# Performance work log

Measured on AMD Instinct MI355X. Metric: run time of the kernel, lower is better.

## Reference

```python
import jax, jax.numpy as jnp
import numpy as np

B, H, W, C, HEADS, WS, SS = 32, 56, 56, 512, 16, 7, 3
HID = 4 * C
N = WS * WS          # tokens per window = 49
NW = (H // WS) * (W // WS)  # windows per image = 64
HD = C // HEADS
SCALE = HD ** -0.5

def _rel_index():
    coords = np.stack(np.meshgrid(np.arange(WS), np.arange(WS), indexing='ij'))
    cf = coords.reshape(2, -1)
    rel = (cf[:, :, None] - cf[:, None, :]).transpose(1, 2, 0)
    rel[..., 0] += WS - 1
    rel[..., 1] += WS - 1
    rel[..., 0] *= 2 * WS - 1
    return rel.sum(-1)  # [N, N]

REL_IDX = _rel_index()

def _attn_mask():
    # standard Swin SW-MSA mask: label 3x3 shifted regions, diff labels -> -100
    img = np.zeros((H, W), dtype=np.float32)
    cnt = 0
    for hs in (slice(0, -WS), slice(-WS, -SS), slice(-SS, None)):
        for ws_ in (slice(0, -WS), slice(-WS, -SS), slice(-SS, None)):
            img[hs, ws_] = cnt
            cnt += 1
    mw = img.reshape(H // WS, WS, W // WS, WS).transpose(0, 2, 1, 3).reshape(NW, N)
    diff = mw[:, None, :] - mw[:, :, None]
    return jnp.asarray(np.where(diff != 0, -100.0, 0.0).astype(np.float32))  # [NW, N, N]

ATTN_MASK = _attn_mask()

def layernorm(x, g, b, eps=1e-5):
    m = jnp.mean(x, -1, keepdims=True)
    v = jnp.mean((x - m) ** 2, -1, keepdims=True)
    return (x - m) * jax.lax.rsqrt(v + eps) * g + b

def setup_inputs():
    key = jax.random.key(0)
    ks = jax.random.split(key, 8)
    f32 = jnp.float32
    return {
        'x': jax.random.normal(ks[0], (B, H * W, C), f32),
        'norm1_g': jnp.ones((C,), f32), 'norm1_b': jnp.zeros((C,), f32),
        'qkv_w': jax.random.normal(ks[1], (3 * C, C), f32) * 0.02,
        'qkv_b': jnp.zeros((3 * C,), f32),
        'rel_bias': jax.random.normal(ks[2], ((2 * WS - 1) ** 2, HEADS), f32) * 0.02,
        'proj_w': jax.random.normal(ks[3], (C, C), f32) * 0.02,
        'proj_b': jnp.zeros((C,), f32),
        'norm2_g': jnp.ones((C,), f32), 'norm2_b': jnp.zeros((C,), f32),
        'mlp_w1': jax.random.normal(ks[4], (HID, C), f32) * 0.02,
        'mlp_b1': jnp.zeros((HID,), f32),
        'mlp_w2': jax.random.normal(ks[5], (C, HID), f32) * 0.02,
        'mlp_b2': jnp.zeros((C,), f32),
    }

def reference(x, norm1_g, norm1_b, qkv_w, qkv_b, rel_bias, proj_w, proj_b,
              norm2_g, norm2_b, mlp_w1, mlp_b1, mlp_w2, mlp_b2):
    skip = x
    h = layernorm(x, norm1_g, norm1_b).reshape(B, H, W, C)
    h = jnp.roll(h, (-SS, -SS), axis=(1, 2))  # cyclic shift
    # window partition -> [B*NW, N, C]
    h = h.reshape(B, H // WS, WS, W // WS, WS, C).transpose(0, 1, 3, 2, 4, 5).reshape(B * NW, N, C)
    qkv = (h @ qkv_w.T + qkv_b).reshape(B * NW, N, 3, HEADS, HD).transpose(2, 0, 3, 1, 4)
    q, k, v = qkv[0] * SCALE, qkv[1], qkv[2]  # [B*NW, HEADS, N, HD]
    attn = jnp.einsum('whnd,whmd->whnm', q, k)
    bias = rel_bias[REL_IDX.reshape(-1)].reshape(N, N, HEADS).transpose(2, 0, 1)
    attn = attn + bias[None]
    attn = attn.reshape(B, NW, HEADS, N, N) + ATTN_MASK[None, :, None]
    attn = jax.nn.softmax(attn, axis=-1).reshape(B * NW, HEADS, N, N)
    h = jnp.einsum('whnm,whmd->whnd', attn, v).transpose(0, 2, 1, 3).reshape(B * NW, N, C)
    h = h @ proj_w.T + proj_b
    # window reverse + reverse cyclic shift
    h = h.reshape(B, H // WS, W // WS, WS, WS, C).transpose(0, 1, 3, 2, 4, 5).reshape(B, H, W, C)
    h = jnp.roll(h, (SS, SS), axis=(1, 2)).reshape(B, H * W, C)
    x = skip + h
    m = layernorm(x, norm2_g, norm2_b)
    m = jax.nn.gelu(m @ mlp_w1.T + mlp_b1, approximate=False) @ mlp_w2.T + mlp_b2
    return x + m
```

## Files before the change

### kernel.cpp

```cpp
#include <hip/hip_runtime.h>
#include <cstdint>
#include <cstddef>

#define DI __device__ __forceinline__

typedef __bf16 bf16_t;
typedef __bf16 bf16x8 __attribute__((ext_vector_type(8)));
typedef float f32x4 __attribute__((ext_vector_type(4)));

static constexpr float SCALE = 0.17677669529663687f;

DI bf16_t f2b(float f) {
  uint32_t u = __builtin_bit_cast(uint32_t, f);
  u += 0x7fffu + ((u >> 16) & 1u);
  return __builtin_bit_cast(bf16_t, (uint16_t)(u >> 16));
}

DI void gld16(const void* g, void* l) {
  __builtin_amdgcn_global_load_lds(
      (const __attribute__((address_space(1))) uint32_t*)g,
      (__attribute__((address_space(3))) uint32_t*)l, 16, 0, 0);
}

__global__ __launch_bounds__(256)
void cvtw(const float* __restrict__ in, bf16_t* __restrict__ out, int n) {
  int i = (blockIdx.x * 256 + threadIdx.x) * 4;
  if (i >= n) return;
  float4 v = *(const float4*)(in + i);
  ushort4 o;
  o.x = __builtin_bit_cast(uint16_t, f2b(v.x));
  o.y = __builtin_bit_cast(uint16_t, f2b(v.y));
  o.z = __builtin_bit_cast(uint16_t, f2b(v.z));
  o.w = __builtin_bit_cast(uint16_t, f2b(v.w));
  *(ushort4*)(out + i) = o;
}

__global__ __launch_bounds__(256)
void bias_pre(const float* __restrict__ rel, float* __restrict__ bf) {
  int idx = blockIdx.x * 256 + threadIdx.x;
  int head = idx >> 12, t1 = (idx >> 6) & 63, t2 = idx & 63;
  float v = -1e30f;
  if (t1 < 49 && t2 < 49) {
    int i1 = t1 / 7, j1 = t1 - i1 * 7, i2 = t2 / 7, j2 = t2 - i2 * 7;
    v = rel[((i1 - i2 + 6) * 13 + (j1 - j2 + 6)) * 16 + head];
  }
  bf[idx] = v;
}

template<bool WIN>
__global__ __launch_bounds__(256)
void ln_kernel(const float* __restrict__ in, const float* __restrict__ g,
               const float* __restrict__ be, bf16_t* __restrict__ out)
{
  const int tid = threadIdx.x;
  const int r = blockIdx.x * 2 + (tid >> 7);
  const int ti = tid & 127;
  long srow;
  if (WIN) {
    int bw = r / 49, t = r - bw * 49;
    int b = bw >> 6, w = bw & 63;
    int wh = w >> 3, ww = w & 7;
    int i = t / 7, j = t - i * 7;
    int hs = wh * 7 + i + 3; if (hs >= 56) hs -= 56;
    int wsr = ww * 7 + j + 3; if (wsr >= 56) wsr -= 56;
    srow = (long)b * 3136 + hs * 56 + wsr;
  } else {
    srow = r;
  }
  const float4 v = *(const float4*)(in + srow * 512 + ti * 4);
  float s = v.x + v.y + v.z + v.w;
  float sq = v.x * v.x + v.y * v.y + v.z * v.z + v.w * v.w;
#pragma unroll
  for (int m = 1; m < 64; m <<= 1) { s += __shfl_xor(s, m); sq += __shfl_xor(sq, m); }
  __shared__ float ls[4], lq[4];
  const int wv = tid >> 6;
  if ((tid & 63) == 0) { ls[wv] = s; lq[wv] = sq; }
  __syncthreads();
  const int rp = (tid >> 7) * 2;
  s = ls[rp] + ls[rp + 1]; sq = lq[rp] + lq[rp + 1];
  const float mean = s * (1.f / 512.f);
  const float rs = rsqrtf(sq * (1.f / 512.f) - mean * mean + 1e-5f);
  const float4 gg = *(const float4*)(g + ti * 4);
  const float4 bb = *(const float4*)(be + ti * 4);
  ushort4 o;
  o.x = __builtin_bit_cast(uint16_t, f2b((v.x - mean) * rs * gg.x + bb.x));
  o.y = __builtin_bit_cast(uint16_t, f2b((v.y - mean) * rs * gg.y + bb.y));
  o.z = __builtin_bit_cast(uint16_t, f2b((v.z - mean) * rs * gg.z + bb.z));
  o.w = __builtin_bit_cast(uint16_t, f2b((v.w - mean) * rs * gg.w + bb.w));
  *(ushort4*)(out + (long)r * 512 + ti * 4) = o;
}

#define MFMA16(a, b, c) __builtin_amdgcn_mfma_f32_16x16x32_bf16((a), (b), (c), 0, 0, 0)

template<int EPI>
DI void epi_store(int grow, int gcol, float v, const float* extra,
                  void* out0, void* out1v, void* out2v)
{
  long obase = 0;
  if (EPI == 0) {
    int bwi = grow / 49, t_ = grow - bwi * 49;
    obase = ((long)bwi * 784 + t_) * 32;
  } else if (EPI == 1) {
    int bwi = grow / 49, t_ = grow - bwi * 49;
    int b = bwi >> 6, w = bwi & 63;
    int wh = w >> 3, ww = w & 7;
    int i = t_ / 7, jj = t_ - i * 7;
    int hs = wh * 7 + i + 3; if (hs >= 56) hs -= 56;
    int wsr = ww * 7 + jj + 3; if (wsr >= 56) wsr -= 56;
    obase = ((long)b * 3136 + hs * 56 + wsr) * 512;
  } else if (EPI == 2) {
    obase = (long)grow * 2048;
  } else {
    obase = (long)grow * 512;
  }
  if (EPI == 0) {
    int part = gcol >> 9, head = (gcol >> 5) & 15, d = gcol & 31;
    if (part == 0) v *= SCALE;
    bf16_t* dst = (bf16_t*)(part == 0 ? out0 : (part == 1 ? out1v : out2v));
    dst[obase + (long)head * 1568 + d] = f2b(v);
  } else if (EPI == 1) {
    ((float*)out0)[obase + gcol] = v + extra[obase + gcol];
  } else if (EPI == 2) {
    float m2 = v * v;
    float z = v * fmaf(0.07135481627f, m2, 1.59576912161f);
    float e = __expf(z);
    float rr = __builtin_amdgcn_rcpf(e + 1.0f);
    ((bf16_t*)out0)[obase + gcol] = f2b(fmaf(-v, rr, v));
  } else {
    ((float*)out0)[obase + gcol] = v + extra[obase + gcol];
  }
}

template<int EPI, int NBN, int NT>
__global__ __launch_bounds__(512, 2)
void gemmM(const bf16_t* __restrict__ A, const bf16_t* __restrict__ Bw,
           const float* __restrict__ bias, const float* __restrict__ extra,
           void* __restrict__ out0, void* __restrict__ out1v, void* __restrict__ out2v)
{
  constexpr int K = NT * 32;
  __shared__ __align__(128) bf16_t ldsA[2][8192];
  __shared__ __align__(128) bf16_t ldsB[4][8192];
  const int tid = threadIdx.x, lane = tid & 63, wave = tid >> 6;
  const int xcd = blockIdx.x & 7, j = blockIdx.x >> 3;
  const int m0 = xcd * 49;
  constexpr int ntileX = 49 * NBN;
  const int tiles = (ntileX - j + 31) >> 5;

  const int arow = tid >> 1, ac = (tid & 1) * 2;
  const int awb0 = arow * 64 + ((ac ^ ((arow >> 1) & 3)) << 4);
  const int awb1 = arow * 64 + (((ac + 1) ^ ((arow >> 1) & 3)) << 4);
  const int bsrow = tid >> 2;
  const int bchunk = (tid & 3) ^ ((bsrow >> 1) & 3);

  int ktS = 0, tS = j;
  const bf16_t* pA = A + ((size_t)(m0 + tS / NBN) * 256 + arow) * K + ac * 8;
  const bf16_t* pB = Bw + ((size_t)(tS % NBN) * 256 + bsrow) * K + bchunk * 8;

  struct QA { uint4 x, y; };
  QA qa0, qa1, qa2, qa3;

#define ADV() do { \
    if (++ktS == NT) { \
      ktS = 0; tS += 32; if (tS >= ntileX) tS = j; \
      pA = A + ((size_t)(m0 + tS / NBN) * 256 + arow) * K + ac * 8; \
      pB = Bw + ((size_t)(tS % NBN) * 256 + bsrow) * K + bchunk * 8; \
    } \
  } while (0)

#define STEPOPS(QI, TGT) do { \
    QI.x = *(const uint4*)(pA + ktS * 32); \
    QI.y = *(const uint4*)(pA + ktS * 32 + 8); \
    gld16(pB + ktS * 32, &ldsB[TGT][tid * 8]); \
    gld16(pB + ktS * 32 + (size_t)128 * K, &ldsB[TGT][tid * 8 + 4096]); \
    ADV(); \
  } while (0)

#define COMMIT(QC, BUF) do { \
    *(uint4*)((char*)&ldsA[BUF][0] + awb0) = QC.x; \
    *(uint4*)((char*)&ldsA[BUF][0] + awb1) = QC.y; \
  } while (0)

  const int fr = lane & 15, fkc = lane >> 4;
  const int wr = wave >> 2, wc = wave & 3;
  const int slotq = (fkc ^ ((fr >> 1) & 3)) << 3;
  const int aoff = (wr * 128 + fr) * 32 + slotq;
  const int boff = (wc * 64 + fr) * 32 + slotq;

  f32x4 acc[8][4] = {};

  STEPOPS(qa0, 0); STEPOPS(qa1, 1); STEPOPS(qa2, 2);
  asm volatile("s_waitcnt vmcnt(8)");
  __builtin_amdgcn_sched_barrier(0);
  COMMIT(qa0, 0);
  asm volatile("s_waitcnt lgkmcnt(0)");
  __builtin_amdgcn_s_barrier();
  __builtin_amdgcn_sched_barrier(0);

#define PH(P, QI, QC) do { \
    bf16x8 bq0 = *(const bf16x8*)&ldsB[(P) & 3][boff]; \
    bf16x8 bq1 = *(const bf16x8*)&ldsB[(P) & 3][boff + 512]; \
    bf16x8 bq2 = *(const bf16x8*)&ldsB[(P) & 3][boff + 1024]; \
    bf16x8 bq3 = *(const bf16x8*)&ldsB[(P) & 3][boff + 1536]; \
    bf16x8 a0 = *(const bf16x8*)&ldsA[(P) & 1][aoff]; \
    bf16x8 a1 = *(const bf16x8*)&ldsA[(P) & 1][aoff + 512]; \
    bf16x8 a2 = *(const bf16x8*)&ldsA[(P) & 1][aoff + 1024]; \
    bf16x8 a3 = *(const bf16x8*)&ldsA[(P) & 1][aoff + 1536]; \
    STEPOPS(QI, ((P) + 3) & 3); \
    asm volatile("s_waitcnt lgkmcnt(0)"); \
    __builtin_amdgcn_sched_barrier(0); \
    __builtin_amdgcn_s_setprio(1); \
    acc[0][0] = MFMA16(a0, bq0, acc[0][0]); acc[0][1] = MFMA16(a0, bq1, acc[0][1]); \
    acc[0][2] = MFMA16(a0, bq2, acc[0][2]); acc[0][3] = MFMA16(a0, bq3, acc[0][3]); \
    acc[1][0] = MFMA16(a1, bq0, acc[1][0]); acc[1][1] = MFMA16(a1, bq1, acc[1][1]); \
    acc[1][2] = MFMA16(a1, bq2, acc[1][2]); acc[1][3] = MFMA16(a1, bq3, acc[1][3]); \
    acc[2][0] = MFMA16(a2, bq0, acc[2][0]); acc[2][1] = MFMA16(a2, bq1, acc[2][1]); \
    acc[2][2] = MFMA16(a2, bq2, acc[2][2]); acc[2][3] = MFMA16(a2, bq3, acc[2][3]); \
    acc[3][0] = MFMA16(a3, bq0, acc[3][0]); acc[3][1] = MFMA16(a3, bq1, acc[3][1]); \
    acc[3][2] = MFMA16(a3, bq2, acc[3][2]); acc[3][3] = MFMA16(a3, bq3, acc[3][3]); \
    a0 = *(const bf16x8*)&ldsA[(P) & 1][aoff + 2048]; \
    a1 = *(const bf16x8*)&ldsA[(P) & 1][aoff + 2560]; \
    a2 = *(const bf16x8*)&ldsA[(P) & 1][aoff + 3072]; \
    a3 = *(const bf16x8*)&ldsA[(P) & 1][aoff + 3584]; \
    asm volatile("s_waitcnt lgkmcnt(0)"); \
    __builtin_amdgcn_sched_barrier(0); \
    acc[4][0] = MFMA16(a0, bq0, acc[4][0]); acc[4][1] = MFMA16(a0, bq1, acc[4][1]); \
    acc[4][2] = MFMA16(a0, bq2, acc[4][2]); acc[4][3] = MFMA16(a0, bq3, acc[4][3]); \
    acc[5][0] = MFMA16(a1, bq0, acc[5][0]); acc[5][1] = MFMA16(a1, bq1, acc[5][1]); \
    acc[5][2] = MFMA16(a1, bq2, acc[5][2]); acc[5][3] = MFMA16(a1, bq3, acc[5][3]); \
    acc[6][0] = MFMA16(a2, bq0, acc[6][0]); acc[6][1] = MFMA16(a2, bq1, acc[6][1]); \
    acc[6][2] = MFMA16(a2, bq2, acc[6][2]); acc[6][3] = MFMA16(a2, bq3, acc[6][3]); \
    acc[7][0] = MFMA16(a3, bq0, acc[7][0]); acc[7][1] = MFMA16(a3, bq1, acc[7][1]); \
    acc[7][2] = MFMA16(a3, bq2, acc[7][2]); acc[7][3] = MFMA16(a3, bq3, acc[7][3]); \
    __builtin_amdgcn_s_setprio(0); \
    __builtin_amdgcn_sched_barrier(0); \
    asm volatile("s_waitcnt vmcnt(8)"); \
    __builtin_amdgcn_sched_barrier(0); \
    COMMIT(QC, ((P) + 1) & 1); \
    asm volatile("s_waitcnt lgkmcnt(0)"); \
    __builtin_amdgcn_s_barrier(); \
    __builtin_amdgcn_sched_barrier(0); \
  } while (0)

  const int rq = fkc * 4;

  for (int t = 0; t < tiles; ++t) {
    const int tauC = j + t * 32;
    const int bmC = m0 + tauC / NBN;
    const int bnC = tauC % NBN;
#pragma unroll 1
    for (int it = 0; it < NT / 4; ++it) {
      PH(0, qa3, qa1);
      PH(1, qa0, qa2);
      PH(2, qa1, qa3);
      PH(3, qa2, qa0);
    }
    float bs[4];
#pragma unroll
    for (int n = 0; n < 4; ++n) bs[n] = bias[bnC * 256 + wc * 64 + n * 16 + fr];
#pragma unroll
    for (int m = 0; m < 8; ++m)
#pragma unroll
      for (int jj = 0; jj < 4; ++jj) {
        const int grow = bmC * 256 + wr * 128 + m * 16 + rq + jj;
#pragma unroll
        for (int n = 0; n < 4; ++n) {
          const int gcol = bnC * 256 + wc * 64 + n * 16 + fr;
          epi_store<EPI>(grow, gcol, acc[m][n][jj] + bs[n], extra, out0, out1v, out2v);
        }
      }
#pragma unroll
    for (int m = 0; m < 8; ++m)
#pragma unroll
      for (int n = 0; n < 4; ++n) acc[m][n] = (f32x4){0.f, 0.f, 0.f, 0.f};
  }
#undef PH
#undef COMMIT
#undef STEPOPS
#undef ADV
}

__global__ __launch_bounds__(256)
void attn_kernel(const bf16_t* __restrict__ qb, const bf16_t* __restrict__ kb,
                 const bf16_t* __restrict__ vb, const float* __restrict__ biasf,
                 bf16_t* __restrict__ aout)
{
  __shared__ bf16_t Q[64 * 32];
  __shared__ bf16_t Kl[64 * 32];
  __shared__ bf16_t Vt[32 * 64];
  __shared__ bf16_t Pl[4][16 * 64];
  const int bid = blockIdx.x;
  const int bw = bid >> 4, head = bid & 15;
  const int tid = threadIdx.x, lane = tid & 63, wave = tid >> 6;
  {
    uint4 z = {0u, 0u, 0u, 0u};
    *(uint4*)&Q[tid * 8] = z;
    *(uint4*)&Kl[tid * 8] = z;
    *(uint4*)&Vt[tid * 8] = z;
  }
  __syncthreads();
  const bf16_t* qsrc = qb + (long)bid * (49 * 32);
  const bf16_t* ksrc = kb + (long)bid * (49 * 32);
  const bf16_t* vsrc = vb + (long)bid * (49 * 32);
  if (tid < 196) {
    *(uint4*)&Q[tid * 8] = *(const uint4*)(qsrc + tid * 8);
    *(uint4*)&Kl[tid * 8] = *(const uint4*)(ksrc + tid * 8);
  }
  for (int e = tid; e < 1568; e += 256) {
    int t = e >> 5, d = e & 31;
    Vt[d * 64 + t] = vsrc[e];
  }
  __syncthreads();
  const int fr = lane & 15, fk = (lane >> 4) * 8, rq = (lane >> 4) * 4;
  bf16x8 aq = *(const bf16x8*)&Q[(wave * 16 + fr) * 32 + fk];
  f32x4 s[4];
#pragma unroll
  for (int n = 0; n < 4; ++n) {
    bf16x8 bk = *(const bf16x8*)&Kl[(n * 16 + fr) * 32 + fk];
    f32x4 z = {0.f, 0.f, 0.f, 0.f};
    s[n] = __builtin_amdgcn_mfma_f32_16x16x32_bf16(aq, bk, z, 0, 0, 0);
  }
  const int w = bw & 63;
  const bool wh7 = ((w >> 3) == 7), ww7 = ((w & 7) == 7);
  const float* bh = biasf + head * 4096;
#pragma unroll
  for (int j = 0; j < 4; ++j) {
    const int row = wave * 16 + rq + j;
    int i1 = row / 7, j1 = row - i1 * 7;
    bool b1h = wh7 && (i1 >= 4), b1w = ww7 && (j1 >= 4);
    float pv[4];
    float mx = -3.0e38f;
#pragma unroll
    for (int n = 0; n < 4; ++n) {
      const int col = n * 16 + fr;
      float v = s[n][j] + bh[row * 64 + col];
      if (wh7 || ww7) {
        int i2 = col / 7, j2 = col - i2 * 7;
        bool b2h = wh7 && (i2 >= 4), b2w = ww7 && (j2 >= 4);
        if ((b1h != b2h) || (b1w != b2w)) v -= 100.f;
      }
      pv[n] = v;
      mx = fmaxf(mx, v);
    }
#pragma unroll
    for (int msk = 1; msk < 16; msk <<= 1) mx = fmaxf(mx, __shfl_xor(mx, msk));
    float sm = 0.f;
#pragma unroll
    for (int n = 0; n < 4; ++n) { pv[n] = __expf(pv[n] - mx); sm += pv[n]; }
#pragma unroll
    for (int msk = 1; msk < 16; msk <<= 1) sm += __shfl_xor(sm, msk);
    const float inv = 1.f / sm;
#pragma unroll
    for (int n = 0; n < 4; ++n)
      Pl[wave][(rq + j) * 64 + n * 16 + fr] = f2b(pv[n] * inv);
  }
  __syncthreads();
  f32x4 o[2] = {};
#pragma unroll
  for (int kk = 0; kk < 2; ++kk) {
    bf16x8 pa = *(const bf16x8*)&Pl[wave][fr * 64 + kk * 32 + fk];
#pragma unroll
    for (int dt = 0; dt < 2; ++dt) {
      bf16x8 vv = *(const bf16x8*)&Vt[(dt * 16 + fr) * 64 + kk * 32 + fk];
      o[dt] = __builtin_amdgcn_mfma_f32_16x16x32_bf16(pa, vv, o[dt], 0, 0, 0);
    }
  }
#pragma unroll
  for (int j = 0; j < 4; ++j) {
    const int t1 = wave * 16 + rq + j;
    if (t1 < 49) {
      bf16_t* dst = aout + ((long)bw * 49 + t1) * 512 + head * 32;
      dst[fr] = f2b(o[0][j]);
      dst[16 + fr] = f2b(o[1][j]);
    }
  }
}

extern "C" void kernel_launch(void* const* d_in, const int* in_sizes, int n_in,
                              void* d_out, int out_size, void* d_ws, size_t ws_size,
                              hipStream_t stream)
{
  const float* x      = (const float*)d_in[0];
  const float* n1g    = (const float*)d_in[1];
  const float* n1b    = (const float*)d_in[2];
  const float* qkv_w  = (const float*)d_in[3];
  const float* qkv_b  = (const float*)d_in[4];
  const float* rel    = (const float*)d_in[5];
  const float* proj_w = (const float*)d_in[6];
  const float* proj_b = (const float*)d_in[7];
  const float* n2g    = (const float*)d_in[8];
  const float* n2b    = (const float*)d_in[9];
  const float* w1     = (const float*)d_in[10];
  const float* b1     = (const float*)d_in[11];
  const float* w2     = (const float*)d_in[12];
  const float* b2     = (const float*)d_in[13];

  char* ws = (char*)d_ws;
  bf16_t* Wqkv  = (bf16_t*)(ws + 0);
  bf16_t* Wproj = (bf16_t*)(ws + 1572864);
  bf16_t* Wm1   = (bf16_t*)(ws + 2097152);
  bf16_t* Wm2   = (bf16_t*)(ws + 4194304);
  float*  biasf = (float*)(ws + 6291456);
  const size_t ABYTES = (size_t)100352 * 512 * 2;
  const size_t P1 = 8388608;
  const size_t P2 = P1 + ABYTES + 1048576;
  bf16_t* xw      = (bf16_t*)(ws + P1);
  bf16_t* qbuf    = (bf16_t*)(ws + P2);
  bf16_t* kbuf    = (bf16_t*)(ws + P2 + ABYTES);
  bf16_t* vbuf    = (bf16_t*)(ws + P2 + 2 * ABYTES);
  bf16_t* attnout = xw;
  bf16_t* h2      = xw;
  bf16_t* hidden  = qbuf;

  cvtw<<<768, 256, 0, stream>>>(qkv_w, Wqkv, 1536 * 512);
  cvtw<<<256, 256, 0, stream>>>(proj_w, Wproj, 512 * 512);
  cvtw<<<1024, 256, 0, stream>>>(w1, Wm1, 2048 * 512);
  cvtw<<<1024, 256, 0, stream>>>(w2, Wm2, 512 * 2048);
  bias_pre<<<256, 256, 0, stream>>>(rel, biasf);

  ln_kernel<true><<<50176, 256, 0, stream>>>(x, n1g, n1b, xw);
  gemmM<0, 6, 16><<<256, 512, 0, stream>>>(xw, Wqkv, qkv_b, nullptr,
                                           qbuf, kbuf, vbuf);
  attn_kernel<<<32768, 256, 0, stream>>>(qbuf, kbuf, vbuf, biasf, attnout);
  gemmM<1, 2, 16><<<256, 512, 0, stream>>>(attnout, Wproj, proj_b, x,
                                           d_out, nullptr, nullptr);
  ln_kernel<false><<<50176, 256, 0, stream>>>((const float*)d_out, n2g, n2b, h2);
  gemmM<2, 8, 16><<<256, 512, 0, stream>>>(h2, Wm1, b1, nullptr,
                                           hidden, nullptr, nullptr);
  gemmM<3, 2, 64><<<256, 512, 0, stream>>>(hidden, Wm2, b2, (const float*)d_out,
                                           d_out, nullptr, nullptr);
}
```

Before: 1.628 ms.

## Replace templated GEMM with runtime-parameterised kernel using fixed column tile per block

```diff
diff --git a/kernel.cpp b/kernel.cpp
--- a/kernel.cpp
+++ b/kernel.cpp
@@ -14,12 +14,6 @@
   uint32_t u = __builtin_bit_cast(uint32_t, f);
   u += 0x7fffu + ((u >> 16) & 1u);
   return __builtin_bit_cast(bf16_t, (uint16_t)(u >> 16));
-}
-
-DI void gld16(const void* g, void* l) {
-  __builtin_amdgcn_global_load_lds(
-      (const __attribute__((address_space(1))) uint32_t*)g,
-      (__attribute__((address_space(3))) uint32_t*)l, 16, 0, 0);
 }
 
 __global__ __launch_bounds__(256)
@@ -131,53 +125,57 @@
   }
 }
 
-template<int EPI, int NBN, int NT>
-__global__ __launch_bounds__(512, 2)
-void gemmM(const bf16_t* __restrict__ A, const bf16_t* __restrict__ Bw,
+__global__ __launch_bounds__(512, 1)
+void gemmQ(const bf16_t* __restrict__ A, const bf16_t* __restrict__ Bw,
            const float* __restrict__ bias, const float* __restrict__ extra,
-           void* __restrict__ out0, void* __restrict__ out1v, void* __restrict__ out2v)
+           void* __restrict__ out0, void* __restrict__ out1v, void* __restrict__ out2v,
+           const int K, const int NBN, const int EPI)
 {
-  constexpr int K = NT * 32;
-  __shared__ __align__(128) bf16_t ldsA[2][8192];
-  __shared__ __align__(128) bf16_t ldsB[4][8192];
+  __shared__ __align__(128) bf16_t lds[4][2][8192];
   const int tid = threadIdx.x, lane = tid & 63, wave = tid >> 6;
+  const int NT = K >> 5;
+
   const int xcd = blockIdx.x & 7, j = blockIdx.x >> 3;
+  const int G = 32 / NBN;
+  if (j >= G * NBN) return;
+  const int bmo = j / NBN;
+  const int bn = j - bmo * NBN;
   const int m0 = xcd * 49;
-  constexpr int ntileX = 49 * NBN;
-  const int tiles = (ntileX - j + 31) >> 5;
-
-  const int arow = tid >> 1, ac = (tid & 1) * 2;
-  const int awb0 = arow * 64 + ((ac ^ ((arow >> 1) & 3)) << 4);
-  const int awb1 = arow * 64 + (((ac + 1) ^ ((arow >> 1) & 3)) << 4);
-  const int bsrow = tid >> 2;
-  const int bchunk = (tid & 3) ^ ((bsrow >> 1) & 3);
-
-  int ktS = 0, tS = j;
-  const bf16_t* pA = A + ((size_t)(m0 + tS / NBN) * 256 + arow) * K + ac * 8;
-  const bf16_t* pB = Bw + ((size_t)(tS % NBN) * 256 + bsrow) * K + bchunk * 8;
-
-  struct QA { uint4 x, y; };
-  QA qa0, qa1, qa2, qa3;
-
-#define ADV() do { \
+  const int tiles = (49 - bmo + G - 1) / G;
+
+  const int srow = tid >> 2, slot = tid & 3;
+  const int chunk = slot ^ ((srow >> 1) & 3);
+  const size_t rowK = (size_t)128 * K;
+  const size_t strideA = (size_t)G * 256 * K;
+
+  const bf16_t* const pA0 = A + ((size_t)(m0 + bmo) * 256 + srow) * K + chunk * 8;
+  const bf16_t* const pB0 = Bw + ((size_t)bn * 256 + srow) * K + chunk * 8;
+  const bf16_t* pAs = pA0;
+  int ktS = 0, tSS = 0;
+
+  struct Q16 { uint4 alo, ahi, blo, bhi; };
+  Q16 qa0, qa1, qa2, qa3;
+
+#define ISSUE(Q) do { \
+    const bf16_t* _pa = pAs + ktS * 32; \
+    const bf16_t* _pb = pB0 + ktS * 32; \
+    Q.alo = *(const uint4*)_pa; \
+    Q.ahi = *(const uint4*)(_pa + rowK); \
+    Q.blo = *(const uint4*)_pb; \
+    Q.bhi = *(const uint4*)(_pb + rowK); \
     if (++ktS == NT) { \
-      ktS = 0; tS += 32; if (tS >= ntileX) tS = j; \
-      pA = A + ((size_t)(m0 + tS / NBN) * 256 + arow) * K + ac * 8; \
-      pB = Bw + ((size_t)(tS % NBN) * 256 + bsrow) * K + bchunk * 8; \
+      ktS = 0; \
+      if (++tSS >= tiles) { tSS = 0; pAs = pA0; } else pAs += strideA; \
     } \
   } while (0)
 
-#define STEPOPS(QI, TGT) do { \
-    QI.x = *(const uint4*)(pA + ktS * 32); \
-    QI.y = *(const uint4*)(pA + ktS * 32 + 8); \
-    gld16(pB + ktS * 32, &ldsB[TGT][tid * 8]); \
-    gld16(pB + ktS * 32 + (size_t)128 * K, &ldsB[TGT][tid * 8 + 4096]); \
-    ADV(); \
-  } while (0)
-
-#define COMMIT(QC, BUF) do { \
-    *(uint4*)((char*)&ldsA[BUF][0] + awb0) = QC.x; \
-    *(uint4*)((char*)&ldsA[BUF][0] + awb1) = QC.y; \
+#define COMMIT(Q, BUF) do { \
+    char* _bA = (char*)&lds[BUF][0][0]; \
+    char* _bB = (char*)&lds[BUF][1][0]; \
+    *(uint4*)(_bA + tid * 16) = Q.alo; \
+    *(uint4*)(_bA + tid * 16 + 8192) = Q.ahi; \
+    *(uint4*)(_bB + tid * 16) = Q.blo; \
+    *(uint4*)(_bB + tid * 16 + 8192) = Q.bhi; \
   } while (0)
 
   const int fr = lane & 15, fkc = lane >> 4;
@@ -188,7 +186,7 @@
 
   f32x4 acc[8][4] = {};
 
-  STEPOPS(qa0, 0); STEPOPS(qa1, 1); STEPOPS(qa2, 2);
+  ISSUE(qa0); ISSUE(qa1); ISSUE(qa2);
   asm volatile("s_waitcnt vmcnt(8)");
   __builtin_amdgcn_sched_barrier(0);
   COMMIT(qa0, 0);
@@ -197,66 +195,44 @@
   __builtin_amdgcn_sched_barrier(0);
 
 #define PH(P, QI, QC) do { \
-    bf16x8 bq0 = *(const bf16x8*)&ldsB[(P) & 3][boff]; \
-    bf16x8 bq1 = *(const bf16x8*)&ldsB[(P) & 3][boff + 512]; \
-    bf16x8 bq2 = *(const bf16x8*)&ldsB[(P) & 3][boff + 1024]; \
-    bf16x8 bq3 = *(const bf16x8*)&ldsB[(P) & 3][boff + 1536]; \
-    bf16x8 a0 = *(const bf16x8*)&ldsA[(P) & 1][aoff]; \
-    bf16x8 a1 = *(const bf16x8*)&ldsA[(P) & 1][aoff + 512]; \
-    bf16x8 a2 = *(const bf16x8*)&ldsA[(P) & 1][aoff + 1024]; \
-    bf16x8 a3 = *(const bf16x8*)&ldsA[(P) & 1][aoff + 1536]; \
-    STEPOPS(QI, ((P) + 3) & 3); \
+    bf16x8 af[8], bq[4]; \
+    _Pragma("unroll") \
+    for (int m = 0; m < 8; ++m) af[m] = *(const bf16x8*)&lds[P][0][aoff + m * 512]; \
+    _Pragma("unroll") \
+    for (int n = 0; n < 4; ++n) bq[n] = *(const bf16x8*)&lds[P][1][boff + n * 512]; \
+    ISSUE(QI); \
     asm volatile("s_waitcnt lgkmcnt(0)"); \
     __builtin_amdgcn_sched_barrier(0); \
     __builtin_amdgcn_s_setprio(1); \
-    acc[0][0] = MFMA16(a0, bq0, acc[0][0]); acc[0][1] = MFMA16(a0, bq1, acc[0][1]); \
-    acc[0][2] = MFMA16(a0, bq2, acc[0][2]); acc[0][3] = MFMA16(a0, bq3, acc[0][3]); \
-    acc[1][0] = MFMA16(a1, bq0, acc[1][0]); acc[1][1] = MFMA16(a1, bq1, acc[1][1]); \
-    acc[1][2] = MFMA16(a1, bq2, acc[1][2]); acc[1][3] = MFMA16(a1, bq3, acc[1][3]); \
-    acc[2][0] = MFMA16(a2, bq0, acc[2][0]); acc[2][1] = MFMA16(a2, bq1, acc[2][1]); \
-    acc[2][2] = MFMA16(a2, bq2, acc[2][2]); acc[2][3] = MFMA16(a2, bq3, acc[2][3]); \
-    acc[3][0] = MFMA16(a3, bq0, acc[3][0]); acc[3][1] = MFMA16(a3, bq1, acc[3][1]); \
-    acc[3][2] = MFMA16(a3, bq2, acc[3][2]); acc[3][3] = MFMA16(a3, bq3, acc[3][3]); \
-    a0 = *(const bf16x8*)&ldsA[(P) & 1][aoff + 2048]; \
-    a1 = *(const bf16x8*)&ldsA[(P) & 1][aoff + 2560]; \
-    a2 = *(const bf16x8*)&ldsA[(P) & 1][aoff + 3072]; \
-    a3 = *(const bf16x8*)&ldsA[(P) & 1][aoff + 3584]; \
-    asm volatile("s_waitcnt lgkmcnt(0)"); \
-    __builtin_amdgcn_sched_barrier(0); \
-    acc[4][0] = MFMA16(a0, bq0, acc[4][0]); acc[4][1] = MFMA16(a0, bq1, acc[4][1]); \
-    acc[4][2] = MFMA16(a0, bq2, acc[4][2]); acc[4][3] = MFMA16(a0, bq3, acc[4][3]); \
-    acc[5][0] = MFMA16(a1, bq0, acc[5][0]); acc[5][1] = MFMA16(a1, bq1, acc[5][1]); \
-    acc[5][2] = MFMA16(a1, bq2, acc[5][2]); acc[5][3] = MFMA16(a1, bq3, acc[5][3]); \
-    acc[6][0] = MFMA16(a2, bq0, acc[6][0]); acc[6][1] = MFMA16(a2, bq1, acc[6][1]); \
-    acc[6][2] = MFMA16(a2, bq2, acc[6][2]); acc[6][3] = MFMA16(a2, bq3, acc[6][3]); \
-    acc[7][0] = MFMA16(a3, bq0, acc[7][0]); acc[7][1] = MFMA16(a3, bq1, acc[7][1]); \
-    acc[7][2] = MFMA16(a3, bq2, acc[7][2]); acc[7][3] = MFMA16(a3, bq3, acc[7][3]); \
+    _Pragma("unroll") \
+    for (int m = 0; m < 8; ++m) \
+      _Pragma("unroll") \
+      for (int n = 0; n < 4; ++n) \
+        acc[m][n] = MFMA16(af[m], bq[n], acc[m][n]); \
     __builtin_amdgcn_s_setprio(0); \
     __builtin_amdgcn_sched_barrier(0); \
     asm volatile("s_waitcnt vmcnt(8)"); \
     __builtin_amdgcn_sched_barrier(0); \
-    COMMIT(QC, ((P) + 1) & 1); \
+    COMMIT(QC, (P + 1) & 3); \
     asm volatile("s_waitcnt lgkmcnt(0)"); \
     __builtin_amdgcn_s_barrier(); \
     __builtin_amdgcn_sched_barrier(0); \
   } while (0)
 
   const int rq = fkc * 4;
+  float bs[4];
+#pragma unroll
+  for (int n = 0; n < 4; ++n) bs[n] = bias[bn * 256 + wc * 64 + n * 16 + fr];
 
   for (int t = 0; t < tiles; ++t) {
-    const int tauC = j + t * 32;
-    const int bmC = m0 + tauC / NBN;
-    const int bnC = tauC % NBN;
+    const int bmC = m0 + bmo + t * G;
 #pragma unroll 1
-    for (int it = 0; it < NT / 4; ++it) {
+    for (int k4 = 0; k4 < NT; k4 += 4) {
       PH(0, qa3, qa1);
       PH(1, qa0, qa2);
       PH(2, qa1, qa3);
       PH(3, qa2, qa0);
     }
-    float bs[4];
-#pragma unroll
-    for (int n = 0; n < 4; ++n) bs[n] = bias[bnC * 256 + wc * 64 + n * 16 + fr];
 #pragma unroll
     for (int m = 0; m < 8; ++m)
 #pragma unroll
@@ -264,8 +240,12 @@
         const int grow = bmC * 256 + wr * 128 + m * 16 + rq + jj;
 #pragma unroll
         for (int n = 0; n < 4; ++n) {
-          const int gcol = bnC * 256 + wc * 64 + n * 16 + fr;
-          epi_store<EPI>(grow, gcol, acc[m][n][jj] + bs[n], extra, out0, out1v, out2v);
+          const int gcol = bn * 256 + wc * 64 + n * 16 + fr;
+          const float v = acc[m][n][jj] + bs[n];
+          if (EPI == 0)      epi_store<0>(grow, gcol, v, extra, out0, out1v, out2v);
+          else if (EPI == 1) epi_store<1>(grow, gcol, v, extra, out0, out1v, out2v);
+          else if (EPI == 2) epi_store<2>(grow, gcol, v, extra, out0, out1v, out2v);
+          else               epi_store<3>(grow, gcol, v, extra, out0, out1v, out2v);
         }
       }
 #pragma unroll
@@ -275,8 +255,7 @@
   }
 #undef PH
 #undef COMMIT
-#undef STEPOPS
-#undef ADV
+#undef ISSUE
 }
 
 __global__ __launch_bounds__(256)
@@ -418,14 +397,14 @@
   bias_pre<<<256, 256, 0, stream>>>(rel, biasf);
 
   ln_kernel<true><<<50176, 256, 0, stream>>>(x, n1g, n1b, xw);
-  gemmM<0, 6, 16><<<256, 512, 0, stream>>>(xw, Wqkv, qkv_b, nullptr,
-                                           qbuf, kbuf, vbuf);
+  gemmQ<<<256, 512, 0, stream>>>(xw, Wqkv, qkv_b, nullptr,
+                                 qbuf, kbuf, vbuf, 512, 6, 0);
   attn_kernel<<<32768, 256, 0, stream>>>(qbuf, kbuf, vbuf, biasf, attnout);
-  gemmM<1, 2, 16><<<256, 512, 0, stream>>>(attnout, Wproj, proj_b, x,
-                                           d_out, nullptr, nullptr);
+  gemmQ<<<256, 512, 0, stream>>>(attnout, Wproj, proj_b, x,
+                                 d_out, nullptr, nullptr, 512, 2, 1);
   ln_kernel<false><<<50176, 256, 0, stream>>>((const float*)d_out, n2g, n2b, h2);
-  gemmM<2, 8, 16><<<256, 512, 0, stream>>>(h2, Wm1, b1, nullptr,
-                                           hidden, nullptr, nullptr);
-  gemmM<3, 2, 64><<<256, 512, 0, stream>>>(hidden, Wm2, b2, (const float*)d_out,
-                                           d_out, nullptr, nullptr);
-}
+  gemmQ<<<256, 512, 0, stream>>>(h2, Wm1, b1, nullptr,
+                                 hidden, nullptr, nullptr, 512, 8, 2);
+  gemmQ<<<256, 512, 0, stream>>>(hidden, Wm2, b2, (const float*)d_out,
+                                 d_out, nullptr, nullptr, 2048, 2, 3);
+}
```

Result: slower. 3.180 ms (+95.3%).
